# Performance work log

Measured on AMD Instinct MI355X. Metric: run time of the kernel, lower is better.

## Reference

```python
import jax, jax.numpy as jnp
import numpy as np

B, C, DEPTH, HEADS, D2, NC = 16, 768, 12, 12, 2, 1000
P, IMG = 16, 224
GH = IMG // P          # 14 patches per side
NP = GH * GH           # 196 patches
HD = C // HEADS        # 64
SCALE = HD ** -0.5
EPS = 1e-6

def _ln(x, w, b):
    m = x.mean(-1, keepdims=True)
    v = ((x - m) ** 2).mean(-1, keepdims=True)
    return (x - m) / jnp.sqrt(v + EPS) * w + b

def _mlp(x, f1w, f1b, f2w, f2b):
    return jax.nn.gelu(x @ f1w.T + f1b, approximate=False) @ f2w.T + f2b

def _head_mix(attn, w, b):  # nn.Linear(num_heads, num_heads) applied over head axis
    return jnp.einsum('bhnm,gh->bgnm', attn, w) + b[None, :, None, None]

def setup_inputs():
    keys = iter(jax.random.split(jax.random.key(0), 80))
    def rp(*shape, s=0.02):
        return jax.random.normal(next(keys), shape, jnp.float32) * s
    return {
        'x': jax.random.normal(next(keys), (B, 3, IMG, IMG), jnp.float32),
        'patch_w': rp(C, 3 * P * P), 'patch_b': rp(C),
        'cls_token': rp(1, 1, C), 'pos_embed': rp(1, NP, C),
        # talking-head blocks, params stacked over DEPTH
        'n1w': jnp.ones((DEPTH, C)), 'n1b': jnp.zeros((DEPTH, C)),
        'qkvw': rp(DEPTH, 3 * C, C), 'qkvb': rp(DEPTH, 3 * C),
        'plw': rp(DEPTH, HEADS, HEADS), 'plb': rp(DEPTH, HEADS),
        'pww': rp(DEPTH, HEADS, HEADS), 'pwb': rp(DEPTH, HEADS),
        'projw': rp(DEPTH, C, C), 'projb': rp(DEPTH, C),
        'n2w': jnp.ones((DEPTH, C)), 'n2b': jnp.zeros((DEPTH, C)),
        'f1w': rp(DEPTH, 4 * C, C), 'f1b': rp(DEPTH, 4 * C),
        'f2w': rp(DEPTH, C, 4 * C), 'f2b': rp(DEPTH, C),
        'g1': jnp.full((DEPTH, C), 1e-4, jnp.float32), 'g2': jnp.full((DEPTH, C), 1e-4, jnp.float32),
        # class-attention token-only blocks, stacked over D2
        'tn1w': jnp.ones((D2, C)), 'tn1b': jnp.zeros((D2, C)),
        'tqw': rp(D2, C, C), 'tqb': rp(D2, C),
        'tkw': rp(D2, C, C), 'tkb': rp(D2, C),
        'tvw': rp(D2, C, C), 'tvb': rp(D2, C),
        'tprojw': rp(D2, C, C), 'tprojb': rp(D2, C),
        'tn2w': jnp.ones((D2, C)), 'tn2b': jnp.zeros((D2, C)),
        'tf1w': rp(D2, 4 * C, C), 'tf1b': rp(D2, 4 * C),
        'tf2w': rp(D2, C, 4 * C), 'tf2b': rp(D2, C),
        'tg1': jnp.full((D2, C), 1e-4, jnp.float32), 'tg2': jnp.full((D2, C), 1e-4, jnp.float32),
        'normw': jnp.ones((C,)), 'normb': jnp.zeros((C,)),
        'headw': rp(NC, C), 'headb': rp(NC),
    }

def reference(x, patch_w, patch_b, cls_token, pos_embed,
              n1w, n1b, qkvw, qkvb, plw, plb, pww, pwb, projw, projb,
              n2w, n2b, f1w, f1b, f2w, f2b, g1, g2,
              tn1w, tn1b, tqw, tqb, tkw, tkb, tvw, tvb, tprojw, tprojb,
              tn2w, tn2b, tf1w, tf1b, tf2w, tf2b, tg1, tg2,
              normw, normb, headw, headb):
    # patch embed: non-overlapping 16x16 conv expressed as patch-flatten + matmul
    p = x.reshape(B, 3, GH, P, GH, P).transpose(0, 2, 4, 1, 3, 5).reshape(B, NP, 3 * P * P)
    h = p @ patch_w.T + patch_b + pos_embed  # [B, NP, C]

    def th_block(hx, pr):
        a_n1w, a_n1b, a_qkvw, a_qkvb, a_plw, a_plb, a_pww, a_pwb, a_pw, a_pb, a_n2w, a_n2b, a_f1w, a_f1b, a_f2w, a_f2b, a_g1, a_g2 = pr
        y = _ln(hx, a_n1w, a_n1b)
        qkv = (y @ a_qkvw.T + a_qkvb).reshape(B, NP, 3, HEADS, HD).transpose(2, 0, 3, 1, 4)
        q, k, v = qkv[0] * SCALE, qkv[1], qkv[2]
        attn = jnp.einsum('bhnd,bhmd->bhnm', q, k)
        attn = _head_mix(attn, a_plw, a_plb)        # pre-softmax talking heads
        attn = jax.nn.softmax(attn, axis=-1)
        attn = _head_mix(attn, a_pww, a_pwb)        # post-softmax talking heads
        o = jnp.einsum('bhnm,bhmd->bnhd', attn, v).reshape(B, NP, C)
        hx = hx + a_g1 * (o @ a_pw.T + a_pb)
        hx = hx + a_g2 * _mlp(_ln(hx, a_n2w, a_n2b), a_f1w, a_f1b, a_f2w, a_f2b)
        return hx, None

    h, _ = jax.lax.scan(th_block, h, (n1w, n1b, qkvw, qkvb, plw, plb, pww, pwb, projw, projb, n2w, n2b, f1w, f1b, f2w, f2b, g1, g2))

    cls = jnp.broadcast_to(cls_token, (B, 1, C))

    def ca_block(cl, pr):
        b_n1w, b_n1b, b_qw, b_qb, b_kw, b_kb, b_vw, b_vb, b_pw, b_pb, b_n2w, b_n2b, b_f1w, b_f1b, b_f2w, b_f2b, b_g1, b_g2 = pr
        u = _ln(jnp.concatenate([cl, h], axis=1), b_n1w, b_n1b)  # [B, 1+NP, C]
        q = (u[:, 0] @ b_qw.T + b_qb).reshape(B, HEADS, 1, HD) * SCALE
        k = (u @ b_kw.T + b_kb).reshape(B, 1 + NP, HEADS, HD).transpose(0, 2, 1, 3)
        v = (u @ b_vw.T + b_vb).reshape(B, 1 + NP, HEADS, HD).transpose(0, 2, 1, 3)
        attn = jax.nn.softmax(jnp.einsum('bhqd,bhmd->bhqm', q, k), axis=-1)
        o = jnp.einsum('bhqm,bhmd->bqhd', attn, v).reshape(B, 1, C)
        cl = cl + b_g1 * (o @ b_pw.T + b_pb)
        cl = cl + b_g2 * _mlp(_ln(cl, b_n2w, b_n2b), b_f1w, b_f1b, b_f2w, b_f2b)
        return cl, None

    cls, _ = jax.lax.scan(ca_block, cls, (tn1w, tn1b, tqw, tqb, tkw, tkb, tvw, tvb, tprojw, tprojb, tn2w, tn2b, tf1w, tf1b, tf2w, tf2b, tg1, tg2))

    z = _ln(jnp.concatenate([cls, h], axis=1), normw, normb)
    return z[:, 0] @ headw.T + headb  # [B, num_classes]
```

## Files before the change

### kernel.cpp

```cpp
#include <hip/hip_runtime.h>
#include <hip/hip_bf16.h>

using bf16 = __hip_bfloat16;
typedef short short8 __attribute__((ext_vector_type(8)));
typedef float floatx4 __attribute__((ext_vector_type(4)));

#define B_   16
#define C_   768
#define NP_  196
#define H_   12
#define NPNP 38416

static __device__ __forceinline__ float b2f(bf16 v) { return __bfloat162float(v); }
static __device__ __forceinline__ unsigned short f2bfbits(float f) {
    bf16 t = __float2bfloat16(f);
    return *(unsigned short*)&t;
}

template<int BM, int BN, int WM, int WN, int WFP>
__global__ __launch_bounds__(256)
void k_mgemm(const bf16* __restrict__ A, long long sAo, long long sAi, int ABI, int lda,
             const void* __restrict__ W, long long sWo, long long sWi, int WBI, int ldw,
             char* __restrict__ Cb, long long sCo, long long sCi, int CBI, int ldc,
             const float* __restrict__ bias, const float* __restrict__ resg,
             int M, int N, int K, float scale, int act, int outbf)
{
    constexpr int FM = BM / (16 * WM);
    constexpr int FN = BN / (16 * WN);
    constexpr int ACH = (BM * 4 + 255) / 256;
    constexpr int WCH = (BN * 4 + 255) / 256;

    __shared__ unsigned short As[2 * BM * 40];
    __shared__ unsigned short Ws[2 * BN * 40];

    const int z = blockIdx.z;
    const long long aoff = (long long)(z / ABI) * sAo + (long long)(z % ABI) * sAi;
    const long long woff = (long long)(z / WBI) * sWo + (long long)(z % WBI) * sWi;
    const unsigned short* Ag = (const unsigned short*)A + aoff;

    const int tid = threadIdx.x;
    const int lane = tid & 63, w = tid >> 6;
    const int wm = w / WN, wn = w % WN;
    const int p = lane & 15, q = lane >> 4;
    const int bm = blockIdx.y * BM, bn = blockIdx.x * BN;

    short8  aR[ACH];
    short8  wR[WCH];
    floatx4 w0R[WCH], w1R[WCH];

    auto loadAB = [&](int k0) {
#pragma unroll
        for (int i = 0; i < ACH; i++) {
            int c = tid + 256 * i;
            if (c < BM * 4) {
                int r = c >> 2, off = (c & 3) * 8;
                int am = bm + r; am = (am < M) ? am : (M - 1);
                aR[i] = *(const short8*)(Ag + (size_t)am * lda + k0 + off);
            }
        }
#pragma unroll
        for (int i = 0; i < WCH; i++) {
            int c = tid + 256 * i;
            if (c < BN * 4) {
                int r = c >> 2, off = (c & 3) * 8;
                int wr = bn + r; wr = (wr < N) ? wr : (N - 1);
                if constexpr (WFP) {
                    const float* wp = (const float*)W + woff + (size_t)wr * ldw + k0 + off;
                    w0R[i] = *(const floatx4*)wp;
                    w1R[i] = *(const floatx4*)(wp + 4);
                } else {
                    wR[i] = *(const short8*)((const unsigned short*)W + woff
                                             + (size_t)wr * ldw + k0 + off);
                }
            }
        }
    };

    auto storeLDS = [&](int buf) {
        unsigned short* Ab = As + buf * (BM * 40);
        unsigned short* Wb = Ws + buf * (BN * 40);
#pragma unroll
        for (int i = 0; i < ACH; i++) {
            int c = tid + 256 * i;
            if (c < BM * 4) {
                int r = c >> 2, off = (c & 3) * 8;
                *(short8*)(&Ab[r * 40 + off]) = aR[i];
            }
        }
#pragma unroll
        for (int i = 0; i < WCH; i++) {
            int c = tid + 256 * i;
            if (c < BN * 4) {
                int r = c >> 2, off = (c & 3) * 8;
                if constexpr (WFP) {
                    unsigned short* d = &Wb[r * 40 + off];
#pragma unroll
                    for (int j = 0; j < 4; j++) d[j]     = f2bfbits(w0R[i][j]);
#pragma unroll
                    for (int j = 0; j < 4; j++) d[4 + j] = f2bfbits(w1R[i][j]);
                } else {
                    *(short8*)(&Wb[r * 40 + off]) = wR[i];
                }
            }
        }
    };

    floatx4 acc[FM][FN] = {};

    loadAB(0);
    storeLDS(0);
    if (32 < K) loadAB(32);
    asm volatile("s_waitcnt lgkmcnt(0)" ::: "memory");
    __builtin_amdgcn_s_barrier();

    int cur = 0;
    for (int k0 = 0; k0 < K; k0 += 32) {
        const unsigned short* Ab = As + cur * (BM * 40);
        const unsigned short* Wb = Ws + cur * (BN * 40);
        short8 af[FM], wf[FN];
#pragma unroll
        for (int i = 0; i < FM; i++)
            af[i] = *(const short8*)(&Ab[(wm * (BM / WM) + i * 16 + p) * 40 + q * 8]);
#pragma unroll
        for (int j = 0; j < FN; j++)
            wf[j] = *(const short8*)(&Wb[(wn * (BN / WN) + j * 16 + p) * 40 + q * 8]);
        __builtin_amdgcn_s_setprio(1);
#pragma unroll
        for (int i = 0; i < FM; i++)
#pragma unroll
            for (int j = 0; j < FN; j++)
                acc[i][j] = __builtin_amdgcn_mfma_f32_16x16x32_bf16(af[i], wf[j], acc[i][j], 0, 0, 0);
        __builtin_amdgcn_s_setprio(0);
        if (k0 + 32 < K) {
            storeLDS(cur ^ 1);
            if (k0 + 64 < K) loadAB(k0 + 64);
            asm volatile("s_waitcnt lgkmcnt(0)" ::: "memory");
            __builtin_amdgcn_s_barrier();
        }
        cur ^= 1;
    }

    const long long coff = (long long)(z / CBI) * sCo + (long long)(z % CBI) * sCi;
    float* Cf = (float*)Cb + coff;
    bf16*  Ch = (bf16*)Cb + coff;
#pragma unroll
    for (int i = 0; i < FM; i++) {
#pragma unroll
        for (int r = 0; r < 4; r++) {
            int gm = bm + wm * (BM / WM) + i * 16 + q * 4 + r;
            if (gm >= M) continue;
#pragma unroll
            for (int j = 0; j < FN; j++) {
                int gn = bn + wn * (BN / WN) + j * 16 + p;
                if (gn >= N) continue;
                float v = acc[i][j][r] * scale;
                if (bias) v += bias[gn];
                if (act) v = 0.5f * v * (1.0f + erff(v * 0.70710678118654752f));
                if (resg)       Cf[(size_t)gm * ldc + gn] += resg[gn] * v;
                else if (outbf) Ch[(size_t)gm * ldc + gn] = __float2bfloat16(v);
                else            Cf[(size_t)gm * ldc + gn] = v;
            }
        }
    }
}

__global__ __launch_bounds__(256)
void k_patch_gather(const float* __restrict__ x, bf16* __restrict__ p)
{
    int idx = blockIdx.x * 256 + threadIdx.x;
    int k = idx % 768;
    int n = (idx / 768) % NP_;
    int b = idx / (768 * NP_);
    int c = k >> 8, r = k & 255;
    int py = r >> 4, px = r & 15;
    int gy = n / 14, gx = n % 14;
    p[idx] = __float2bfloat16(x[(((size_t)b * 3 + c) * 224 + gy * 16 + py) * 224 + gx * 16 + px]);
}

__global__ __launch_bounds__(256)
void k_addpos(float* __restrict__ h, const float* __restrict__ pos)
{
    int idx = blockIdx.x * 256 + threadIdx.x;
    h[idx] += pos[idx % (NP_ * C_)];
}

__device__ __forceinline__ void ln_row(const float* __restrict__ x,
                                       const float* __restrict__ w,
                                       const float* __restrict__ b,
                                       bf16* __restrict__ y, int t,
                                       float* red, float* stat)
{
    float a0 = x[t], a1 = x[t + 256], a2 = x[t + 512];
    float s = a0 + a1 + a2;
#pragma unroll
    for (int off = 32; off > 0; off >>= 1) s += __shfl_down(s, off);
    if ((t & 63) == 0) red[t >> 6] = s;
    __syncthreads();
    if (t == 0) stat[0] = (red[0] + red[1] + red[2] + red[3]) * (1.f / 768.f);
    __syncthreads();
    float m = stat[0];
    float d0 = a0 - m, d1 = a1 - m, d2 = a2 - m;
    float s2 = d0 * d0 + d1 * d1 + d2 * d2;
#pragma unroll
    for (int off = 32; off > 0; off >>= 1) s2 += __shfl_down(s2, off);
    if ((t & 63) == 0) red[t >> 6] = s2;
    __syncthreads();
    if (t == 0) stat[1] = rsqrtf((red[0] + red[1] + red[2] + red[3]) * (1.f / 768.f) + 1e-6f);
    __syncthreads();
    float r = stat[1];
    y[t]       = __float2bfloat16(d0 * r * w[t]       + b[t]);
    y[t + 256] = __float2bfloat16(d1 * r * w[t + 256] + b[t + 256]);
    y[t + 512] = __float2bfloat16(d2 * r * w[t + 512] + b[t + 512]);
}

__global__ __launch_bounds__(256)
void k_ln(const float* __restrict__ X, const float* __restrict__ w,
          const float* __restrict__ b, bf16* __restrict__ Y)
{
    __shared__ float red[4];
    __shared__ float stat[2];
    int row = blockIdx.x;
    ln_row(X + (size_t)row * C_, w, b, Y + (size_t)row * C_, threadIdx.x, red, stat);
}

__global__ __launch_bounds__(256)
void k_ln_cat(const float* __restrict__ cls, const float* __restrict__ h,
              const float* __restrict__ w, const float* __restrict__ b,
              bf16* __restrict__ Y)
{
    __shared__ float red[4];
    __shared__ float stat[2];
    int row = blockIdx.x;
    int bb = row / 197, tkn = row % 197;
    const float* src = (tkn == 0) ? (cls + (size_t)bb * C_)
                                  : (h + ((size_t)bb * NP_ + (tkn - 1)) * C_);
    ln_row(src, w, b, Y + (size_t)row * C_, threadIdx.x, red, stat);
}

__global__ __launch_bounds__(256)
void k_splitv(const bf16* __restrict__ qkv, bf16* __restrict__ VT)
{
    int idx = blockIdx.x * 256 + threadIdx.x;
    int m = idx % 224;
    int rest = idx / 224;
    int d = rest & 63, zz = rest >> 6;
    int b = zz / H_, hh = zz % H_;
    bf16 v = __float2bfloat16(0.f);
    if (m < NP_) v = qkv[((size_t)b * NP_ + m) * 2304 + 1536 + hh * 64 + d];
    VT[idx] = v;
}

__global__ __launch_bounds__(256)
void k_attn_mix(const float* __restrict__ S, const float* __restrict__ plw,
                const float* __restrict__ plb, const float* __restrict__ pww,
                const float* __restrict__ pwb, bf16* __restrict__ P)
{
    __shared__ float wpre[144], wpost[144], bpre[12], bpost[12];
    __shared__ float red[4][12];
    int tid = threadIdx.x;
    if (tid < 144) { wpre[tid] = plw[tid]; wpost[tid] = pww[tid]; }
    if (tid < 12)  { bpre[tid] = plb[tid]; bpost[tid] = pwb[tid]; }
    __syncthreads();
    int b = blockIdx.x / NP_, n = blockIdx.x % NP_;
    int m = tid;
    bool on = (m < NP_);
    const float* p0 = S + ((size_t)b * H_ * NP_ + n) * NP_ + (on ? m : 0);
    float v[12];
#pragma unroll
    for (int h = 0; h < 12; h++) v[h] = p0[(size_t)h * NPNP];
    float s[12];
#pragma unroll
    for (int g = 0; g < 12; g++) {
        float a = bpre[g];
#pragma unroll
        for (int h = 0; h < 12; h++) a += wpre[g * 12 + h] * v[h];
        s[g] = on ? a : -1e30f;
    }
    int wv = tid >> 6, ln = tid & 63;
    float mx[12];
#pragma unroll
    for (int g = 0; g < 12; g++) {
        float x = s[g];
#pragma unroll
        for (int off = 32; off > 0; off >>= 1) x = fmaxf(x, __shfl_down(x, off));
        mx[g] = x;
    }
    if (ln == 0) {
#pragma unroll
        for (int g = 0; g < 12; g++) red[wv][g] = mx[g];
    }
    __syncthreads();
#pragma unroll
    for (int g = 0; g < 12; g++)
        mx[g] = fmaxf(fmaxf(red[0][g], red[1][g]), fmaxf(red[2][g], red[3][g]));
    __syncthreads();
    float e[12], sm[12];
#pragma unroll
    for (int g = 0; g < 12; g++) {
        e[g] = on ? expf(s[g] - mx[g]) : 0.f;
        float x = e[g];
#pragma unroll
        for (int off = 32; off > 0; off >>= 1) x += __shfl_down(x, off);
        sm[g] = x;
    }
    if (ln == 0) {
#pragma unroll
        for (int g = 0; g < 12; g++) red[wv][g] = sm[g];
    }
    __syncthreads();
#pragma unroll
    for (int g = 0; g < 12; g++) {
        float t = (red[0][g] + red[1][g]) + (red[2][g] + red[3][g]);
        e[g] *= 1.0f / t;
    }
    if (on) {
        size_t base = ((size_t)b * H_ * NP_ + n) * 224 + m;
#pragma unroll
        for (int g = 0; g < 12; g++) {
            float a = bpost[g];
#pragma unroll
            for (int h = 0; h < 12; h++) a += wpost[g * 12 + h] * e[h];
            P[base + (size_t)g * NP_ * 224] = __float2bfloat16(a);
        }
    }
}

__global__ __launch_bounds__(256)
void k_ca_attn(const float* __restrict__ q, const bf16* __restrict__ kb,
               const bf16* __restrict__ vb, bf16* __restrict__ o)
{
    __shared__ float sc[200];
    __shared__ float qs[64];
    __shared__ float inv_s;
    int b = blockIdx.x / H_, hh = blockIdx.x % H_;
    int t = threadIdx.x;
    if (t < 64) qs[t] = q[b * C_ + hh * 64 + t] * 0.125f;
    __syncthreads();
    if (t < 197) {
        const bf16* kp = kb + ((size_t)b * 197 + t) * C_ + hh * 64;
        float s = 0.f;
#pragma unroll 8
        for (int d = 0; d < 64; d++) s += qs[d] * b2f(kp[d]);
        sc[t] = s;
    }
    __syncthreads();
    if (t == 0) {
        float mx = -1e30f;
        for (int m = 0; m < 197; m++) mx = fmaxf(mx, sc[m]);
        float sum = 0.f;
        for (int m = 0; m < 197; m++) { float e = expf(sc[m] - mx); sc[m] = e; sum += e; }
        inv_s = 1.0f / sum;
    }
    __syncthreads();
    if (t < 64) {
        const bf16* vp = vb + (size_t)b * 197 * C_ + hh * 64 + t;
        float acc = 0.f;
        for (int m = 0; m < 197; m++) acc += sc[m] * b2f(vp[(size_t)m * C_]);
        o[b * C_ + hh * 64 + t] = __float2bfloat16(acc * inv_s);
    }
}

__global__ __launch_bounds__(256)
void k_bcast_cls(const float* __restrict__ ct, float* __restrict__ cls)
{
    int i = blockIdx.x * 256 + threadIdx.x;
    if (i < B_ * C_) cls[i] = ct[i % C_];
}

__global__ __launch_bounds__(256)
void k_zero(float* __restrict__ p, int n)
{
    int i = blockIdx.x * 256 + threadIdx.x;
    if (i < n) p[i] = 0.f;
}

extern "C" void kernel_launch(void* const* d_in, const int* in_sizes, int n_in,
                              void* d_out, int out_size, void* d_ws, size_t ws_size,
                              hipStream_t stream)
{
    const float* in_x    = (const float*)d_in[0];
    const float* patch_w = (const float*)d_in[1];
    const float* patch_b = (const float*)d_in[2];
    const float* cls_tok = (const float*)d_in[3];
    const float* pos_emb = (const float*)d_in[4];
    const float* n1w = (const float*)d_in[5],  *n1b = (const float*)d_in[6];
    const float* qkvw = (const float*)d_in[7], *qkvb = (const float*)d_in[8];
    const float* plw = (const float*)d_in[9],  *plb = (const float*)d_in[10];
    const float* pww = (const float*)d_in[11], *pwb = (const float*)d_in[12];
    const float* projw = (const float*)d_in[13], *projb = (const float*)d_in[14];
    const float* n2w = (const float*)d_in[15], *n2b = (const float*)d_in[16];
    const float* f1w = (const float*)d_in[17], *f1b = (const float*)d_in[18];
    const float* f2w = (const float*)d_in[19], *f2b = (const float*)d_in[20];
    const float* g1 = (const float*)d_in[21],  *g2 = (const float*)d_in[22];
    const float* tn1w = (const float*)d_in[23], *tn1b = (const float*)d_in[24];
    const float* tqw = (const float*)d_in[25], *tqb = (const float*)d_in[26];
    const float* tkw = (const float*)d_in[27], *tkb = (const float*)d_in[28];
    const float* tvw = (const float*)d_in[29], *tvb = (const float*)d_in[30];
    const float* tprojw = (const float*)d_in[31], *tprojb = (const float*)d_in[32];
    const float* tn2w = (const float*)d_in[33], *tn2b = (const float*)d_in[34];
    const float* tf1w = (const float*)d_in[35], *tf1b = (const float*)d_in[36];
    const float* tf2w = (const float*)d_in[37], *tf2b = (const float*)d_in[38];
    const float* tg1 = (const float*)d_in[39], *tg2 = (const float*)d_in[40];
    const float* normw = (const float*)d_in[41], *normb = (const float*)d_in[42];
    const float* headw = (const float*)d_in[43], *headb = (const float*)d_in[44];
    (void)in_sizes; (void)n_in; (void)out_size; (void)ws_size;

    const int M = B_ * NP_;
    char* wsb = (char*)d_ws;
    float* h    = (float*)(wsb + 0);
    bf16*  yB   = (bf16*)(wsb + 9633792);
    char*  BIG  = wsb + 14450688;
    bf16*  VT   = (bf16*)(wsb + 53587968);
    bf16*  P    = (bf16*)(wsb + 59092992);
    bf16*  oB   = (bf16*)(wsb + 75952128);
    bf16*  pbuf = (bf16*)BIG;
    bf16*  qkvB = (bf16*)BIG;
    float* S    = (float*)BIG;
    bf16*  hidB = (bf16*)BIG;
    bf16*  u    = (bf16*)BIG;
    bf16*  kbuf = (bf16*)(BIG + 5242880);
    bf16*  vbuf = (bf16*)(BIG + 10485760);
    float* qbuf = (float*)(wsb + 43954176);
    bf16*  ca_o = (bf16*)(wsb + 43954176 + 65536);
    bf16*  clsB = (bf16*)(wsb + 43954176 + 262144);
    bf16*  cmlp = (bf16*)(wsb + 43954176 + 327680);
    float* cls  = (float*)(wsb + 59092992);

    auto mg = [&](int tm, int tn,
                  const bf16* A, long long sAo, long long sAi, int ABI, int lda,
                  const void* Wt, long long sWo, long long sWi, int WBI, int ldw, int wfp,
                  void* Cc, long long sCo, long long sCi, int CBI, int ldc,
                  const float* bias, const float* resg, int Mm, int Nn, int Kk,
                  float scale, int act, int outbf, int batch) {
        dim3 g((Nn + tn - 1) / tn, (Mm + tm - 1) / tm, batch);
#define MGARGS A, sAo, sAi, ABI, lda, Wt, sWo, sWi, WBI, ldw, (char*)Cc, sCo, sCi, CBI, ldc, \
               bias, resg, Mm, Nn, Kk, scale, act, outbf
        if      (tm == 128 && tn == 128 && !wfp) k_mgemm<128,128,2,2,0><<<g,256,0,stream>>>(MGARGS);
        else if (tm ==  64 && tn == 128 &&  wfp) k_mgemm< 64,128,2,2,1><<<g,256,0,stream>>>(MGARGS);
        else if (tm ==  64 && tn ==  64 &&  wfp) k_mgemm< 64, 64,2,2,1><<<g,256,0,stream>>>(MGARGS);
        else if (tm ==  64 && tn ==  64 && !wfp) k_mgemm< 64, 64,2,2,0><<<g,256,0,stream>>>(MGARGS);
        else if (tm ==  16 && tn == 128 &&  wfp) k_mgemm< 16,128,1,4,1><<<g,256,0,stream>>>(MGARGS);
#undef MGARGS
    };

    k_zero<<<(4214784 + 255) / 256, 256, 0, stream>>>((float*)P, 4214784);

    k_patch_gather<<<9408, 256, 0, stream>>>(in_x, pbuf);
    mg(64, 64, pbuf, 0, 0, 1, 768, patch_w, 0, 0, 1, 768, 1, h, 0, 0, 1, 768,
       patch_b, nullptr, M, 768, 768, 1.f, 0, 0, 1);
    k_addpos<<<9408, 256, 0, stream>>>(h, pos_emb);

    for (int L = 0; L < 12; L++) {
        size_t lC = (size_t)L * C_;
        k_ln<<<M, 256, 0, stream>>>(h, n1w + lC, n1b + lC, yB);
        mg(64, 128, yB, 0, 0, 1, 768, qkvw + (size_t)L * 2304 * 768, 0, 0, 1, 768, 1,
           qkvB, 0, 0, 1, 2304, qkvb + (size_t)L * 2304, nullptr,
           M, 2304, 768, 1.f, 0, 1, 1);
        k_splitv<<<10752, 256, 0, stream>>>(qkvB, VT);
        mg(128, 128, qkvB, (long long)NP_ * 2304, 64, H_, 2304,
           qkvB + 768, (long long)NP_ * 2304, 64, H_, 2304, 0,
           S, NPNP, 0, 1, 196, nullptr, nullptr,
           196, 196, 64, 0.125f, 0, 0, 192);
        k_attn_mix<<<M, 256, 0, stream>>>(S, plw + L * 144, plb + L * 12,
                                          pww + L * 144, pwb + L * 12, P);
        mg(64, 64, P, 43904, 0, 1, 224, VT, 14336, 0, 1, 224, 0,
           oB, 150528, 64, H_, 768, nullptr, nullptr,
           196, 64, 224, 1.f, 0, 1, 192);
        mg(64, 64, oB, 0, 0, 1, 768, projw + (size_t)L * 768 * 768, 0, 0, 1, 768, 1,
           h, 0, 0, 1, 768, projb + lC, g1 + lC, M, 768, 768, 1.f, 0, 0, 1);
        k_ln<<<M, 256, 0, stream>>>(h, n2w + lC, n2b + lC, yB);
        mg(64, 128, yB, 0, 0, 1, 768, f1w + (size_t)L * 3072 * 768, 0, 0, 1, 768, 1,
           hidB, 0, 0, 1, 3072, f1b + (size_t)L * 3072, nullptr,
           M, 3072, 768, 1.f, 1, 1, 1);
        mg(64, 64, hidB, 0, 0, 1, 3072, f2w + (size_t)L * 768 * 3072, 0, 0, 1, 3072, 1,
           h, 0, 0, 1, 768, f2b + lC, g2 + lC, M, 768, 3072, 1.f, 0, 0, 1);
    }

    k_bcast_cls<<<48, 256, 0, stream>>>(cls_tok, cls);
    const int Mu = B_ * 197;
    for (int t = 0; t < 2; t++) {
        size_t tC = (size_t)t * C_;
        size_t tCC = (size_t)t * 768 * 768;
        size_t tFC = (size_t)t * 3072 * 768;
        k_ln_cat<<<Mu, 256, 0, stream>>>(cls, h, tn1w + tC, tn1b + tC, u);
        mg(16, 128, u, 0, 0, 1, 197 * 768, tqw + tCC, 0, 0, 1, 768, 1,
           qbuf, 0, 0, 1, 768, tqb + tC, nullptr, B_, 768, 768, 1.f, 0, 0, 1);
        mg(64, 64, u, 0, 0, 1, 768, tkw + tCC, 0, 0, 1, 768, 1,
           kbuf, 0, 0, 1, 768, tkb + tC, nullptr, Mu, 768, 768, 1.f, 0, 1, 1);
        mg(64, 64, u, 0, 0, 1, 768, tvw + tCC, 0, 0, 1, 768, 1,
           vbuf, 0, 0, 1, 768, tvb + tC, nullptr, Mu, 768, 768, 1.f, 0, 1, 1);
        k_ca_attn<<<B_ * H_, 256, 0, stream>>>(qbuf, kbuf, vbuf, ca_o);
        mg(16, 128, ca_o, 0, 0, 1, 768, tprojw + tCC, 0, 0, 1, 768, 1,
           cls, 0, 0, 1, 768, tprojb + tC, tg1 + tC, B_, 768, 768, 1.f, 0, 0, 1);
        k_ln<<<B_, 256, 0, stream>>>(cls, tn2w + tC, tn2b + tC, clsB);
        mg(16, 128, clsB, 0, 0, 1, 768, tf1w + tFC, 0, 0, 1, 768, 1,
           cmlp, 0, 0, 1, 3072, tf1b + (size_t)t * 3072, nullptr,
           B_, 3072, 768, 1.f, 1, 1, 1);
        mg(16, 128, cmlp, 0, 0, 1, 3072, tf2w + tFC, 0, 0, 1, 3072, 1,
           cls, 0, 0, 1, 768, tf2b + tC, tg2 + tC, B_, 768, 3072, 1.f, 0, 0, 1);
    }

    k_ln<<<B_, 256, 0, stream>>>(cls, normw, normb, clsB);
    mg(16, 128, clsB, 0, 0, 1, 768, headw, 0, 0, 1, 768, 1, d_out, 0, 0, 1, 1000,
       headb, nullptr, B_, 1000, 768, 1.f, 0, 0, 1);
}
```

Measured before the change: 4.145 ms.

## Add split-K, XCD swizzle, deeper prefetch, skinny GEMV kernel, contiguous Q/K split

The GEMM kernel gains an XCD-aware block swizzle, optional split-K with atomic accumulation (used for the FC2 residual GEMM), and a two-register-set prefetch that keeps two K tiles in flight. A new wavefront-per-output GEMV kernel replaces the 16-row MFMA GEMMs for the class-token path and head. Q and K are copied into contiguous per-head buffers before the score GEMM. Split-K atomics make the summation order nondeterministic, and the extra copy kernel adds memory traffic.

Result: slower. 4.346 ms (+4.9%).

```diff
diff --git a/kernel.cpp b/kernel.cpp
--- a/kernel.cpp
+++ b/kernel.cpp
@@ -3,6 +3,7 @@
 
 using bf16 = __hip_bfloat16;
 typedef short short8 __attribute__((ext_vector_type(8)));
+typedef short short4v __attribute__((ext_vector_type(4)));
 typedef float floatx4 __attribute__((ext_vector_type(4)));
 
 #define B_   16
@@ -12,10 +13,15 @@
 #define NPNP 38416
 
 static __device__ __forceinline__ float b2f(bf16 v) { return __bfloat162float(v); }
+static __device__ __forceinline__ float bits2f(unsigned short u) {
+    union { unsigned int i; float f; } c; c.i = ((unsigned int)u) << 16; return c.f;
+}
 static __device__ __forceinline__ unsigned short f2bfbits(float f) {
     bf16 t = __float2bfloat16(f);
     return *(unsigned short*)&t;
 }
+
+#define LDS_BARRIER() asm volatile("s_waitcnt lgkmcnt(0)\n\ts_barrier" ::: "memory")
 
 template<int BM, int BN, int WM, int WN, int WFP>
 __global__ __launch_bounds__(256)
@@ -23,7 +29,8 @@
              const void* __restrict__ W, long long sWo, long long sWi, int WBI, int ldw,
              char* __restrict__ Cb, long long sCo, long long sCi, int CBI, int ldc,
              const float* __restrict__ bias, const float* __restrict__ resg,
-             int M, int N, int K, float scale, int act, int outbf)
+             int M, int N, int K, float scale, int act, int outbf,
+             int ksplit, int swz)
 {
     constexpr int FM = BM / (16 * WM);
     constexpr int FN = BN / (16 * WN);
@@ -33,7 +40,23 @@
     __shared__ unsigned short As[2 * BM * 40];
     __shared__ unsigned short Ws[2 * BN * 40];
 
-    const int z = blockIdx.z;
+    int bx = blockIdx.x, by = blockIdx.y;
+    if (swz) {
+        int nx = gridDim.x, ny = gridDim.y;
+        int nwg = nx * ny;
+        int lin = by * nx + bx;
+        int qq = nwg >> 3, rr = nwg & 7;
+        int xcd = lin & 7, idx2 = lin >> 3;
+        int s = (xcd < rr) ? (xcd * (qq + 1) + idx2)
+                           : (rr * (qq + 1) + (xcd - rr) * qq + idx2);
+        bx = s % nx; by = s / nx;
+    }
+
+    const int zz = blockIdx.z;
+    const int z = zz / ksplit, ks = zz % ksplit;
+    const int Ks = K / ksplit;
+    const int kbeg = ks * Ks, kend = kbeg + Ks;
+
     const long long aoff = (long long)(z / ABI) * sAo + (long long)(z % ABI) * sAi;
     const long long woff = (long long)(z / WBI) * sWo + (long long)(z % WBI) * sWi;
     const unsigned short* Ag = (const unsigned short*)A + aoff;
@@ -42,81 +65,74 @@
     const int lane = tid & 63, w = tid >> 6;
     const int wm = w / WN, wn = w % WN;
     const int p = lane & 15, q = lane >> 4;
-    const int bm = blockIdx.y * BM, bn = blockIdx.x * BN;
-
-    short8  aR[ACH];
-    short8  wR[WCH];
-    floatx4 w0R[WCH], w1R[WCH];
-
-    auto loadAB = [&](int k0) {
-#pragma unroll
-        for (int i = 0; i < ACH; i++) {
-            int c = tid + 256 * i;
-            if (c < BM * 4) {
-                int r = c >> 2, off = (c & 3) * 8;
-                int am = bm + r; am = (am < M) ? am : (M - 1);
-                aR[i] = *(const short8*)(Ag + (size_t)am * lda + k0 + off);
-            }
-        }
-#pragma unroll
-        for (int i = 0; i < WCH; i++) {
-            int c = tid + 256 * i;
-            if (c < BN * 4) {
-                int r = c >> 2, off = (c & 3) * 8;
-                int wr = bn + r; wr = (wr < N) ? wr : (N - 1);
-                if constexpr (WFP) {
-                    const float* wp = (const float*)W + woff + (size_t)wr * ldw + k0 + off;
-                    w0R[i] = *(const floatx4*)wp;
-                    w1R[i] = *(const floatx4*)(wp + 4);
-                } else {
-                    wR[i] = *(const short8*)((const unsigned short*)W + woff
-                                             + (size_t)wr * ldw + k0 + off);
-                }
-            }
-        }
-    };
-
-    auto storeLDS = [&](int buf) {
-        unsigned short* Ab = As + buf * (BM * 40);
-        unsigned short* Wb = Ws + buf * (BN * 40);
-#pragma unroll
-        for (int i = 0; i < ACH; i++) {
-            int c = tid + 256 * i;
-            if (c < BM * 4) {
-                int r = c >> 2, off = (c & 3) * 8;
-                *(short8*)(&Ab[r * 40 + off]) = aR[i];
-            }
-        }
-#pragma unroll
-        for (int i = 0; i < WCH; i++) {
-            int c = tid + 256 * i;
-            if (c < BN * 4) {
-                int r = c >> 2, off = (c & 3) * 8;
-                if constexpr (WFP) {
-                    unsigned short* d = &Wb[r * 40 + off];
-#pragma unroll
-                    for (int j = 0; j < 4; j++) d[j]     = f2bfbits(w0R[i][j]);
-#pragma unroll
-                    for (int j = 0; j < 4; j++) d[4 + j] = f2bfbits(w1R[i][j]);
-                } else {
-                    *(short8*)(&Wb[r * 40 + off]) = wR[i];
-                }
-            }
-        }
-    };
+    const int bm = by * BM, bn = bx * BN;
+
+    short8  aR0[ACH], aR1[ACH];
+    short8  wR0[WCH], wR1[WCH];
+    floatx4 w0R0[WCH], w1R0[WCH], w0R1[WCH], w1R1[WCH];
+
+#define LOADAB(aR, wR, w0R, w1R, K0_) do {                                       \
+    _Pragma("unroll")                                                            \
+    for (int i = 0; i < ACH; i++) {                                              \
+        int c = tid + 256 * i;                                                   \
+        if (c < BM * 4) {                                                        \
+            int r = c >> 2, off = (c & 3) * 8;                                   \
+            int am = bm + r; am = (am < M) ? am : (M - 1);                       \
+            aR[i] = *(const short8*)(Ag + (size_t)am * lda + (K0_) + off);       \
+        }                                                                        \
+    }                                                                            \
+    _Pragma("unroll")                                                            \
+    for (int i = 0; i < WCH; i++) {                                              \
+        int c = tid + 256 * i;                                                   \
+        if (c < BN * 4) {                                                        \
+            int r = c >> 2, off = (c & 3) * 8;                                   \
+            int wr = bn + r; wr = (wr < N) ? wr : (N - 1);                       \
+            if constexpr (WFP) {                                                 \
+                const float* wp = (const float*)W + woff + (size_t)wr * ldw + (K0_) + off; \
+                w0R[i] = *(const floatx4*)wp;                                    \
+                w1R[i] = *(const floatx4*)(wp + 4);                              \
+            } else {                                                             \
+                wR[i] = *(const short8*)((const unsigned short*)W + woff         \
+                         + (size_t)wr * ldw + (K0_) + off);                      \
+            }                                                                    \
+        }                                                                        \
+    }                                                                            \
+} while (0)
+
+#define STORELDS(aR, wR, w0R, w1R, BUF_) do {                                    \
+    unsigned short* Ab_ = As + (BUF_) * (BM * 40);                               \
+    unsigned short* Wb_ = Ws + (BUF_) * (BN * 40);                               \
+    _Pragma("unroll")                                                            \
+    for (int i = 0; i < ACH; i++) {                                              \
+        int c = tid + 256 * i;                                                   \
+        if (c < BM * 4) {                                                        \
+            int r = c >> 2, off = (c & 3) * 8;                                   \
+            *(short8*)(&Ab_[r * 40 + off]) = aR[i];                              \
+        }                                                                        \
+    }                                                                            \
+    _Pragma("unroll")                                                            \
+    for (int i = 0; i < WCH; i++) {                                              \
+        int c = tid + 256 * i;                                                   \
+        if (c < BN * 4) {                                                        \
+            int r = c >> 2, off = (c & 3) * 8;                                   \
+            if constexpr (WFP) {                                                 \
+                unsigned short* d = &Wb_[r * 40 + off];                          \
+                _Pragma("unroll")                                                \
+                for (int j = 0; j < 4; j++) d[j]     = f2bfbits(w0R[i][j]);      \
+                _Pragma("unroll")                                                \
+                for (int j = 0; j < 4; j++) d[4 + j] = f2bfbits(w1R[i][j]);      \
+            } else {                                                             \
+                *(short8*)(&Wb_[r * 40 + off]) = wR[i];                          \
+            }                                                                    \
+        }                                                                        \
+    }                                                                            \
+} while (0)
 
     floatx4 acc[FM][FN] = {};
 
-    loadAB(0);
-    storeLDS(0);
-    if (32 < K) loadAB(32);
-    asm volatile("s_waitcnt lgkmcnt(0)" ::: "memory");
-    __builtin_amdgcn_s_barrier();
-
-    int cur = 0;
-    for (int k0 = 0; k0 < K; k0 += 32) {
-        const unsigned short* Ab = As + cur * (BM * 40);
-        const unsigned short* Wb = Ws + cur * (BN * 40);
+    auto compute = [&](int cc) {
+        const unsigned short* Ab = As + cc * (BM * 40);
+        const unsigned short* Wb = Ws + cc * (BN * 40);
         short8 af[FM], wf[FN];
 #pragma unroll
         for (int i = 0; i < FM; i++)
@@ -131,14 +147,35 @@
             for (int j = 0; j < FN; j++)
                 acc[i][j] = __builtin_amdgcn_mfma_f32_16x16x32_bf16(af[i], wf[j], acc[i][j], 0, 0, 0);
         __builtin_amdgcn_s_setprio(0);
-        if (k0 + 32 < K) {
-            storeLDS(cur ^ 1);
-            if (k0 + 64 < K) loadAB(k0 + 64);
-            asm volatile("s_waitcnt lgkmcnt(0)" ::: "memory");
-            __builtin_amdgcn_s_barrier();
+    };
+
+    LOADAB(aR0, wR0, w0R0, w1R0, kbeg);
+    STORELDS(aR0, wR0, w0R0, w1R0, 0);
+    if (kbeg + 32 < kend) LOADAB(aR0, wR0, w0R0, w1R0, kbeg + 32);
+    if (kbeg + 64 < kend) LOADAB(aR1, wR1, w0R1, w1R1, kbeg + 64);
+    LDS_BARRIER();
+
+    int cur = 0;
+    for (int k0 = kbeg; k0 < kend; k0 += 64) {
+        compute(cur);
+        if (k0 + 32 < kend) {
+            STORELDS(aR0, wR0, w0R0, w1R0, cur ^ 1);
+            if (k0 + 96 < kend) LOADAB(aR0, wR0, w0R0, w1R0, k0 + 96);
+            LDS_BARRIER();
         }
         cur ^= 1;
-    }
+        if (k0 + 32 < kend) {
+            compute(cur);
+            if (k0 + 64 < kend) {
+                STORELDS(aR1, wR1, w0R1, w1R1, cur ^ 1);
+                if (k0 + 128 < kend) LOADAB(aR1, wR1, w0R1, w1R1, k0 + 128);
+                LDS_BARRIER();
+            }
+            cur ^= 1;
+        }
+    }
+#undef LOADAB
+#undef STORELDS
 
     const long long coff = (long long)(z / CBI) * sCo + (long long)(z % CBI) * sCi;
     float* Cf = (float*)Cb + coff;
@@ -154,12 +191,72 @@
                 int gn = bn + wn * (BN / WN) + j * 16 + p;
                 if (gn >= N) continue;
                 float v = acc[i][j][r] * scale;
-                if (bias) v += bias[gn];
+                if (bias && ks == 0) v += bias[gn];
                 if (act) v = 0.5f * v * (1.0f + erff(v * 0.70710678118654752f));
-                if (resg)       Cf[(size_t)gm * ldc + gn] += resg[gn] * v;
-                else if (outbf) Ch[(size_t)gm * ldc + gn] = __float2bfloat16(v);
-                else            Cf[(size_t)gm * ldc + gn] = v;
+                if (resg) {
+                    float av = resg[gn] * v;
+                    if (ksplit > 1) atomicAdd(&Cf[(size_t)gm * ldc + gn], av);
+                    else            Cf[(size_t)gm * ldc + gn] += av;
+                } else if (outbf) Ch[(size_t)gm * ldc + gn] = __float2bfloat16(v);
+                else              Cf[(size_t)gm * ldc + gn] = v;
             }
+        }
+    }
+}
+
+__global__ __launch_bounds__(256)
+void k_skinny(const bf16* __restrict__ A, long long lda,
+              const float* __restrict__ W, int ldw,
+              char* __restrict__ Cb, int ldc,
+              const float* __restrict__ bias, const float* __restrict__ resg,
+              int N, int K, float scale, int act, int outbf)
+{
+    __shared__ unsigned short Asl[16 * 256];
+    const int t = threadIdx.x;
+    const int wv = t >> 6, lane = t & 63;
+    const int n = blockIdx.x * 4 + wv;
+
+    float acc[16] = {};
+    for (int p0 = 0; p0 < K; p0 += 256) {
+        {
+            int r = t >> 4, c0 = (t & 15) * 16;
+            const unsigned short* ap = (const unsigned short*)A + (size_t)r * lda + p0 + c0;
+            *(short8*)(&Asl[r * 256 + c0])     = *(const short8*)ap;
+            *(short8*)(&Asl[r * 256 + c0 + 8]) = *(const short8*)(ap + 8);
+        }
+        __syncthreads();
+        floatx4 wvv = *(const floatx4*)(W + (size_t)n * ldw + p0 + lane * 4);
+#pragma unroll
+        for (int m = 0; m < 16; m++) {
+            short4v av = *(const short4v*)(&Asl[m * 256 + lane * 4]);
+            float s = acc[m];
+            s += wvv[0] * bits2f((unsigned short)av[0]);
+            s += wvv[1] * bits2f((unsigned short)av[1]);
+            s += wvv[2] * bits2f((unsigned short)av[2]);
+            s += wvv[3] * bits2f((unsigned short)av[3]);
+            acc[m] = s;
+        }
+        __syncthreads();
+    }
+#pragma unroll
+    for (int m = 0; m < 16; m++) {
+        float s = acc[m];
+#pragma unroll
+        for (int off = 32; off > 0; off >>= 1) s += __shfl_down(s, off);
+        acc[m] = s;
+    }
+    if (lane == 0) {
+        float* Cf = (float*)Cb;
+        bf16*  Ch = (bf16*)Cb;
+        float bs = bias ? bias[n] : 0.f;
+        float rg = resg ? resg[n] : 0.f;
+#pragma unroll
+        for (int m = 0; m < 16; m++) {
+            float v = acc[m] * scale + bs;
+            if (act) v = 0.5f * v * (1.0f + erff(v * 0.70710678118654752f));
+            if (resg)       Cf[(size_t)m * ldc + n] += rg * v;
+            else if (outbf) Ch[(size_t)m * ldc + n] = __float2bfloat16(v);
+            else            Cf[(size_t)m * ldc + n] = v;
         }
     }
 }
@@ -238,6 +335,19 @@
 }
 
 __global__ __launch_bounds__(256)
+void k_splitqk(const bf16* __restrict__ qkv, bf16* __restrict__ Qb, bf16* __restrict__ Kb)
+{
+    int idx = blockIdx.x * 256 + threadIdx.x;
+    int d = idx & 63;
+    int rest = idx >> 6;
+    int n = rest % NP_, zz = rest / NP_;
+    int b = zz / H_, hh = zz % H_;
+    size_t src = ((size_t)b * NP_ + n) * 2304 + hh * 64 + d;
+    Qb[idx] = qkv[src];
+    Kb[idx] = qkv[src + 768];
+}
+
+__global__ __launch_bounds__(256)
 void k_splitv(const bf16* __restrict__ qkv, bf16* __restrict__ VT)
 {
     int idx = blockIdx.x * 256 + threadIdx.x;
@@ -310,8 +420,8 @@
     __syncthreads();
 #pragma unroll
     for (int g = 0; g < 12; g++) {
-        float t = (red[0][g] + red[1][g]) + (red[2][g] + red[3][g]);
-        e[g] *= 1.0f / t;
+        float tt = (red[0][g] + red[1][g]) + (red[2][g] + red[3][g]);
+        e[g] *= 1.0f / tt;
     }
     if (on) {
         size_t base = ((size_t)b * H_ * NP_ + n) * 224 + m;
@@ -410,6 +520,8 @@
     float* h    = (float*)(wsb + 0);
     bf16*  yB   = (bf16*)(wsb + 9633792);
     char*  BIG  = wsb + 14450688;
+    bf16*  Qb   = (bf16*)(wsb + 43954176);
+    bf16*  Kb   = (bf16*)(wsb + 48771072);
     bf16*  VT   = (bf16*)(wsb + 53587968);
     bf16*  P    = (bf16*)(wsb + 59092992);
     bf16*  oB   = (bf16*)(wsb + 75952128);
@@ -431,23 +543,29 @@
                   const void* Wt, long long sWo, long long sWi, int WBI, int ldw, int wfp,
                   void* Cc, long long sCo, long long sCi, int CBI, int ldc,
                   const float* bias, const float* resg, int Mm, int Nn, int Kk,
-                  float scale, int act, int outbf, int batch) {
-        dim3 g((Nn + tn - 1) / tn, (Mm + tm - 1) / tm, batch);
+                  float scale, int act, int outbf, int batch, int ksplit, int swz) {
+        dim3 g((Nn + tn - 1) / tn, (Mm + tm - 1) / tm, batch * ksplit);
 #define MGARGS A, sAo, sAi, ABI, lda, Wt, sWo, sWi, WBI, ldw, (char*)Cc, sCo, sCi, CBI, ldc, \
-               bias, resg, Mm, Nn, Kk, scale, act, outbf
+               bias, resg, Mm, Nn, Kk, scale, act, outbf, ksplit, swz
         if      (tm == 128 && tn == 128 && !wfp) k_mgemm<128,128,2,2,0><<<g,256,0,stream>>>(MGARGS);
         else if (tm ==  64 && tn == 128 &&  wfp) k_mgemm< 64,128,2,2,1><<<g,256,0,stream>>>(MGARGS);
         else if (tm ==  64 && tn ==  64 &&  wfp) k_mgemm< 64, 64,2,2,1><<<g,256,0,stream>>>(MGARGS);
         else if (tm ==  64 && tn ==  64 && !wfp) k_mgemm< 64, 64,2,2,0><<<g,256,0,stream>>>(MGARGS);
-        else if (tm ==  16 && tn == 128 &&  wfp) k_mgemm< 16,128,1,4,1><<<g,256,0,stream>>>(MGARGS);
 #undef MGARGS
     };
 
+    auto sk = [&](const bf16* A, long long lda, const float* Wt, int ldw,
+                  void* Cc, int ldc, const float* bias, const float* resg,
+                  int Nn, int Kk, int act, int outbf) {
+        k_skinny<<<dim3(Nn / 4), 256, 0, stream>>>(A, lda, Wt, ldw, (char*)Cc, ldc,
+                                                   bias, resg, Nn, Kk, 1.f, act, outbf);
+    };
+
     k_zero<<<(4214784 + 255) / 256, 256, 0, stream>>>((float*)P, 4214784);
 
     k_patch_gather<<<9408, 256, 0, stream>>>(in_x, pbuf);
     mg(64, 64, pbuf, 0, 0, 1, 768, patch_w, 0, 0, 1, 768, 1, h, 0, 0, 1, 768,
-       patch_b, nullptr, M, 768, 768, 1.f, 0, 0, 1);
+       patch_b, nullptr, M, 768, 768, 1.f, 0, 0, 1, 1, 1);
     k_addpos<<<9408, 256, 0, stream>>>(h, pos_emb);
 
     for (int L = 0; L < 12; L++) {
@@ -455,25 +573,25 @@
         k_ln<<<M, 256, 0, stream>>>(h, n1w + lC, n1b + lC, yB);
         mg(64, 128, yB, 0, 0, 1, 768, qkvw + (size_t)L * 2304 * 768, 0, 0, 1, 768, 1,
            qkvB, 0, 0, 1, 2304, qkvb + (size_t)L * 2304, nullptr,
-           M, 2304, 768, 1.f, 0, 1, 1);
+           M, 2304, 768, 1.f, 0, 1, 1, 1, 1);
+        k_splitqk<<<9408, 256, 0, stream>>>(qkvB, Qb, Kb);
         k_splitv<<<10752, 256, 0, stream>>>(qkvB, VT);
-        mg(128, 128, qkvB, (long long)NP_ * 2304, 64, H_, 2304,
-           qkvB + 768, (long long)NP_ * 2304, 64, H_, 2304, 0,
+        mg(128, 128, Qb, 12544, 0, 1, 64, Kb, 12544, 0, 1, 64, 0,
            S, NPNP, 0, 1, 196, nullptr, nullptr,
-           196, 196, 64, 0.125f, 0, 0, 192);
+           196, 196, 64, 0.125f, 0, 0, 192, 1, 0);
         k_attn_mix<<<M, 256, 0, stream>>>(S, plw + L * 144, plb + L * 12,
                                           pww + L * 144, pwb + L * 12, P);
         mg(64, 64, P, 43904, 0, 1, 224, VT, 14336, 0, 1, 224, 0,
            oB, 150528, 64, H_, 768, nullptr, nullptr,
-           196, 64, 224, 1.f, 0, 1, 192);
+           196, 64, 224, 1.f, 0, 1, 192, 1, 0);
         mg(64, 64, oB, 0, 0, 1, 768, projw + (size_t)L * 768 * 768, 0, 0, 1, 768, 1,
-           h, 0, 0, 1, 768, projb + lC, g1 + lC, M, 768, 768, 1.f, 0, 0, 1);
+           h, 0, 0, 1, 768, projb + lC, g1 + lC, M, 768, 768, 1.f, 0, 0, 1, 1, 1);
         k_ln<<<M, 256, 0, stream>>>(h, n2w + lC, n2b + lC, yB);
         mg(64, 128, yB, 0, 0, 1, 768, f1w + (size_t)L * 3072 * 768, 0, 0, 1, 768, 1,
            hidB, 0, 0, 1, 3072, f1b + (size_t)L * 3072, nullptr,
-           M, 3072, 768, 1.f, 1, 1, 1);
+           M, 3072, 768, 1.f, 1, 1, 1, 1, 1);
         mg(64, 64, hidB, 0, 0, 1, 3072, f2w + (size_t)L * 768 * 3072, 0, 0, 1, 3072, 1,
-           h, 0, 0, 1, 768, f2b + lC, g2 + lC, M, 768, 3072, 1.f, 0, 0, 1);
+           h, 0, 0, 1, 768, f2b + lC, g2 + lC, M, 768, 3072, 1.f, 0, 0, 1, 2, 1);
     }
 
     k_bcast_cls<<<48, 256, 0, stream>>>(cls_tok, cls);
@@ -483,24 +601,19 @@
         size_t tCC = (size_t)t * 768 * 768;
         size_t tFC = (size_t)t * 3072 * 768;
         k_ln_cat<<<Mu, 256, 0, stream>>>(cls, h, tn1w + tC, tn1b + tC, u);
-        mg(16, 128, u, 0, 0, 1, 197 * 768, tqw + tCC, 0, 0, 1, 768, 1,
-           qbuf, 0, 0, 1, 768, tqb + tC, nullptr, B_, 768, 768, 1.f, 0, 0, 1);
+        sk(u, 197 * 768, tqw + tCC, 768, qbuf, 768, tqb + tC, nullptr, 768, 768, 0, 0);
         mg(64, 64, u, 0, 0, 1, 768, tkw + tCC, 0, 0, 1, 768, 1,
-           kbuf, 0, 0, 1, 768, tkb + tC, nullptr, Mu, 768, 768, 1.f, 0, 1, 1);
+           kbuf, 0, 0, 1, 768, tkb + tC, nullptr, Mu, 768, 768, 1.f, 0, 1, 1, 1, 1);
         mg(64, 64, u, 0, 0, 1, 768, tvw + tCC, 0, 0, 1, 768, 1,
-           vbuf, 0, 0, 1, 768, tvb + tC, nullptr, Mu, 768, 768, 1.f, 0, 1, 1);
+           vbuf, 0, 0, 1, 768, tvb + tC, nullptr, Mu, 768, 768, 1.f, 0, 1, 1, 1, 1);
         k_ca_attn<<<B_ * H_, 256, 0, stream>>>(qbuf, kbuf, vbuf, ca_o);
-        mg(16, 128, ca_o, 0, 0, 1, 768, tprojw + tCC, 0, 0, 1, 768, 1,
-           cls, 0, 0, 1, 768, tprojb + tC, tg1 + tC, B_, 768, 768, 1.f, 0, 0, 1);
+        sk(ca_o, 768, tprojw + tCC, 768, cls, 768, tprojb + tC, tg1 + tC, 768, 768, 0, 0);
         k_ln<<<B_, 256, 0, stream>>>(cls, tn2w + tC, tn2b + tC, clsB);
-        mg(16, 128, clsB, 0, 0, 1, 768, tf1w + tFC, 0, 0, 1, 768, 1,
-           cmlp, 0, 0, 1, 3072, tf1b + (size_t)t * 3072, nullptr,
-           B_, 3072, 768, 1.f, 1, 1, 1);
-        mg(16, 128, cmlp, 0, 0, 1, 3072, tf2w + tFC, 0, 0, 1, 3072, 1,
-           cls, 0, 0, 1, 768, tf2b + tC, tg2 + tC, B_, 768, 3072, 1.f, 0, 0, 1);
+        sk(clsB, 768, tf1w + tFC, 768, cmlp, 3072, tf1b + (size_t)t * 3072, nullptr,
+           3072, 768, 1, 1);
+        sk(cmlp, 3072, tf2w + tFC, 3072, cls, 768, tf2b + tC, tg2 + tC, 768, 3072, 0, 0);
     }
 
     k_ln<<<B_, 256, 0, stream>>>(cls, normw, normb, clsB);
-    mg(16, 128, clsB, 0, 0, 1, 768, headw, 0, 0, 1, 768, 1, d_out, 0, 0, 1, 1000,
-       headb, nullptr, B_, 1000, 768, 1.f, 0, 0, 1);
-}
+    sk(clsB, 768, headw, 768, d_out, 1000, headb, nullptr, 1000, 768, 0, 0);
+}
```
